# Optimization experiments

Hardware: AMD Instinct MI355X
Metric: run time of the kernel (lower is better)

Reference implementation:

```python
import jax, jax.numpy as jnp
import numpy as np

B, N, C = 8, 4096, 320
HEAD, SR = 5, 2
HEAD_DIM = C // HEAD
SCALE = HEAD_DIM ** -0.5
LN_EPS = 1e-5


def setup_inputs() -> dict:
    key = jax.random.key(0)
    ks = jax.random.split(key, 8)
    s = 0.02
    return {
        "x": jax.random.normal(ks[0], (B, N, C), jnp.float32),
        "q_w": jax.random.normal(ks[1], (C, C), jnp.float32) * s,
        "q_b": jnp.zeros((C,), jnp.float32),
        "kv_w": jax.random.normal(ks[2], (C, 2 * C), jnp.float32) * s,
        "kv_b": jnp.zeros((2 * C,), jnp.float32),
        "sr_w": jax.random.normal(ks[3], (SR, SR, C, C), jnp.float32) * s,  # HWIO
        "sr_b": jnp.zeros((C,), jnp.float32),
        "ln_g": jnp.ones((C,), jnp.float32),
        "ln_b": jnp.zeros((C,), jnp.float32),
        "proj_w": jax.random.normal(ks[4], (C, C), jnp.float32) * s,
        "proj_b": jnp.zeros((C,), jnp.float32),
        "H": 64,
        "W": 64,
    }


def reference(x, q_w, q_b, kv_w, kv_b, sr_w, sr_b, ln_g, ln_b, proj_w, proj_b, H, W):
    b, n, c = x.shape
    # q projection -> [B, head, N, d]
    q = (x @ q_w + q_b).reshape(b, n, HEAD, HEAD_DIM).transpose(0, 2, 1, 3)
    # spatial reduction of KV: strided conv (kernel=stride=SR) + LayerNorm
    x_img = x.reshape(b, H, W, c)  # NHWC
    x_ = jax.lax.conv_general_dilated(
        x_img, sr_w, window_strides=(SR, SR), padding="VALID",
        dimension_numbers=("NHWC", "HWIO", "NHWC")) + sr_b
    x_ = x_.reshape(b, -1, c)  # [B, N/SR^2, C]
    mu = jnp.mean(x_, axis=-1, keepdims=True)
    var = jnp.mean(jnp.square(x_ - mu), axis=-1, keepdims=True)
    x_ = (x_ - mu) * jax.lax.rsqrt(var + LN_EPS) * ln_g + ln_b
    # kv projection -> k, v each [B, head, Nkv, d]
    kv = (x_ @ kv_w + kv_b).reshape(b, -1, 2, HEAD, HEAD_DIM)
    k = kv[:, :, 0].transpose(0, 2, 1, 3)
    v = kv[:, :, 1].transpose(0, 2, 1, 3)
    # attention
    attn = jnp.einsum("bhnd,bhmd->bhnm", q, k) * SCALE
    attn = jax.nn.softmax(attn, axis=-1)
    out = jnp.einsum("bhnm,bhmd->bhnd", attn, v)
    out = out.transpose(0, 2, 1, 3).reshape(b, n, c)
    return out @ proj_w + proj_b
```

## Files before the change

### kernel.cpp

```cpp
#include <hip/hip_runtime.h>

typedef __attribute__((ext_vector_type(8))) short bf16x8;
typedef __attribute__((ext_vector_type(4))) short bf16x4;
typedef __attribute__((ext_vector_type(4))) float f32x4;
typedef __attribute__((ext_vector_type(2))) float f32x2;
typedef __attribute__((ext_vector_type(2))) unsigned u32x2;
typedef __attribute__((ext_vector_type(4))) unsigned u32x4;

#define DEVI static __device__ __forceinline__
#define AS1 __attribute__((address_space(1)))
#define AS3 __attribute__((address_space(3)))

DEVI unsigned short f2bf(float f) {
  unsigned u = __builtin_bit_cast(unsigned, f);
  return (unsigned short)((u + 0x7FFFu + ((u >> 16) & 1u)) >> 16);
}

DEVI unsigned pkbf(float a, float b) {
#if __has_builtin(__builtin_amdgcn_cvt_pk_bf16_f32)
  return __builtin_bit_cast(unsigned, __builtin_amdgcn_cvt_pk_bf16_f32(a, b));
#else
  return (unsigned)f2bf(a) | ((unsigned)f2bf(b) << 16);
#endif
}

DEVI float fast_exp2(float x) {
#if __has_builtin(__builtin_amdgcn_exp2f)
  return __builtin_amdgcn_exp2f(x);
#else
  return exp2f(x);
#endif
}

DEVI void gl_lds16(const unsigned short* g, unsigned short* l) {
  __builtin_amdgcn_global_load_lds((const AS1 unsigned int*)g, (AS3 unsigned int*)l, 16, 0, 0);
}

DEVI size_t frag_off(int row, int k, int KG) {
  return ((size_t)(row >> 4) * KG + (k >> 3)) * 128 + (row & 15) * 8 + (k & 7);
}

__global__ __launch_bounds__(256)
void k_prep(const float* __restrict__ x, unsigned short* __restrict__ xf) {
  __shared__ __align__(16) unsigned short L[20480];
  const int t = threadIdx.x;
  const size_t base = (size_t)blockIdx.x * 64 * 320;
#pragma unroll
  for (int i = 0; i < 10; i++) {
    int c = i * 256 + t;
    const float* p = x + base + (size_t)c * 8;
    f32x4 a = ((const f32x4*)p)[0], b = ((const f32x4*)p)[1];
    u32x4 pk = {pkbf(a[0], a[1]), pkbf(a[2], a[3]), pkbf(b[0], b[1]), pkbf(b[2], b[3])};
    int r = c / 40, g = c - r * 40;
    int gidx = ((r >> 4) * 40 + g) * 16 + (r & 15);
    int sidx = gidx ^ ((gidx >> 4) & 7);
    *(u32x4*)(L + sidx * 8) = pk;
  }
  __syncthreads();
  unsigned short* outb = xf + base;
#pragma unroll
  for (int i = 0; i < 10; i++) {
    int o = i * 256 + t;
    int sidx = o ^ ((o >> 4) & 7);
    *(u32x4*)(outb + (size_t)o * 8) = *(const u32x4*)(L + sidx * 8);
  }
}

__global__ __launch_bounds__(256)
void k_transpose_all(const float* __restrict__ q_w, const float* __restrict__ kv_w,
                     const float* __restrict__ proj_w, const float* __restrict__ sr_w,
                     unsigned short* __restrict__ Wq, unsigned short* __restrict__ Wkv,
                     unsigned short* __restrict__ Wp, unsigned short* __restrict__ Wsr) {
  const float* src; unsigned short* dst; int K, N;
  switch (blockIdx.z) {
    case 0:  src = q_w;    dst = Wq;  K = 320;  N = 320; break;
    case 1:  src = kv_w;   dst = Wkv; K = 320;  N = 640; break;
    case 2:  src = proj_w; dst = Wp;  K = 320;  N = 320; break;
    default: src = sr_w;   dst = Wsr; K = 1280; N = 320; break;
  }
  if ((int)blockIdx.x >= (K >> 5) || (int)blockIdx.y >= (N >> 5)) return;
  const int KG = K >> 3;
  __shared__ float tile[32][33];
  const int k0 = blockIdx.x * 32, n0 = blockIdx.y * 32;
  const int tx = threadIdx.x, ty = threadIdx.y;
#pragma unroll
  for (int i = 0; i < 4; i++)
    tile[ty + i * 8][tx] = src[(size_t)(k0 + ty + i * 8) * N + n0 + tx];
  __syncthreads();
#pragma unroll
  for (int i = 0; i < 4; i++) {
    int n = n0 + ty + i * 8, k = k0 + tx;
    dst[frag_off(n, k, KG)] = f2bf(tile[tx][ty + i * 8]);
  }
}

__global__ __launch_bounds__(256)
void k_ln(const float* __restrict__ xc, const float* __restrict__ gam,
          const float* __restrict__ bet, unsigned short* __restrict__ xr) {
  const int row = blockIdx.x * 4 + (threadIdx.x >> 6);
  const int l = threadIdx.x & 63;
  const float* p = xc + (size_t)row * 320;
  float s = 0.f, ss = 0.f;
#pragma unroll
  for (int i = 0; i < 5; i++) { float v = p[l + 64 * i]; s += v; ss += v * v; }
#pragma unroll
  for (int o = 1; o < 64; o <<= 1) { s += __shfl_xor(s, o); ss += __shfl_xor(ss, o); }
  float mu = s * (1.f / 320.f);
  float var = ss * (1.f / 320.f) - mu * mu;
  float rstd = rsqrtf(var + 1e-5f);
  if (l < 40) {
    f32x4 a = ((const f32x4*)(p + l * 8))[0], b = ((const f32x4*)(p + l * 8))[1];
    f32x4 ga = ((const f32x4*)(gam + l * 8))[0], gb = ((const f32x4*)(gam + l * 8))[1];
    f32x4 ba = ((const f32x4*)(bet + l * 8))[0], bb = ((const f32x4*)(bet + l * 8))[1];
    f32x4 ya, yb;
#pragma unroll
    for (int j = 0; j < 4; j++) {
      ya[j] = (a[j] - mu) * rstd * ga[j] + ba[j];
      yb[j] = (b[j] - mu) * rstd * gb[j] + bb[j];
    }
    u32x4 pk = {pkbf(ya[0], ya[1]), pkbf(ya[2], ya[3]), pkbf(yb[0], yb[1]), pkbf(yb[2], yb[3])};
    *(u32x4*)(xr + ((size_t)((row >> 4) * 40 + l)) * 128 + (row & 15) * 8) = pk;
  }
}

template <int MT, int AK, int EPI, int NSEG>
__global__ __launch_bounds__(256)
void k_gemm(const unsigned short* __restrict__ A, const unsigned short* __restrict__ W,
            const float* __restrict__ bias, void* __restrict__ outp, void* __restrict__ outp2,
            float oscale) {
  __shared__ __align__(16) unsigned short Bl[20480];
  const int t = threadIdx.x, w = t >> 6, ln = t & 63, lr = ln & 15, lq = ln >> 4;
  const int m0 = blockIdx.x * (MT * 64), n0 = blockIdx.y * 64;

  f32x4 acc[MT][4];
#pragma unroll
  for (int i = 0; i < MT; i++)
#pragma unroll
    for (int j = 0; j < 4; j++) acc[i][j] = (f32x4){0.f, 0.f, 0.f, 0.f};

  int crt[MT], crow[MT];
  if (AK == 1) {
#pragma unroll
    for (int mi = 0; mi < MT; mi++) {
      int gm = m0 + (w * MT + mi) * 16;
      int b = gm >> 10, p = gm & 1023, oy = p >> 5, ox0 = p & 31;
      crt[mi] = b * 256 + ((2 * oy) * 64 + 2 * ox0) >> 4;
      crow[mi] = 0;
      (void)crow[mi];
    }
  }

#pragma unroll
  for (int seg = 0; seg < NSEG; seg++) {
    const int kh = seg >> 1, kw = seg & 1;
    if (seg) __syncthreads();
    if (AK == 0) {
      const unsigned short* Ws = W + ((size_t)(n0 >> 4) * 40) * 128;
#pragma unroll
      for (int j = 0; j < 10; j++)
        gl_lds16(Ws + (size_t)(j * 4 + w) * 512 + ln * 8, Bl + (j * 4 + w) * 512);
    } else {
      const unsigned short* Wt = W + ((size_t)((n0 >> 4) + w) * 160 + seg * 40) * 128;
#pragma unroll
      for (int j = 0; j < 10; j++)
        gl_lds16(Wt + (size_t)j * 512 + ln * 8, Bl + w * 5120 + j * 512);
    }
    __syncthreads();

#pragma unroll
    for (int ks = 0; ks < 10; ks++) {
      bf16x8 af[MT], bfr[4];
#pragma unroll
      for (int mi = 0; mi < MT; mi++) {
        if (AK == 0) {
          af[mi] = *(const bf16x8*)(
              A + ((size_t)((m0 >> 4) + w * MT + mi) * 40 + ks * 4 + lq) * 128 + lr * 8);
        } else {
          int gm = m0 + (w * MT + mi) * 16;
          int b = gm >> 10, p = gm & 1023, oy = p >> 5, ox0 = p & 31;
          int r0 = (2 * oy + kh) * 64 + 2 * ox0 + kw;
          int brt = b * 256 + (r0 >> 4);
          af[mi] = *(const bf16x8*)(
              A + ((size_t)(brt + (lr >> 3)) * 40 + ks * 4 + lq) * 128 +
              (kw + 2 * (lr & 7)) * 8);
        }
      }
#pragma unroll
      for (int ni = 0; ni < 4; ni++)
        bfr[ni] = *(const bf16x8*)(Bl + ((ni * 40) + ks * 4 + lq) * 128 + lr * 8);
#pragma unroll
      for (int mi = 0; mi < MT; mi++)
#pragma unroll
        for (int ni = 0; ni < 4; ni++)
          acc[mi][ni] =
              __builtin_amdgcn_mfma_f32_16x16x32_bf16(af[mi], bfr[ni], acc[mi][ni], 0, 0, 0);
    }
  }

  if (EPI == 0) {
    unsigned short* out = (unsigned short*)outp;
    const int h = n0 >> 6;
#pragma unroll
    for (int mi = 0; mi < MT; mi++)
#pragma unroll
      for (int ni = 0; ni < 4; ni++)
#pragma unroll
        for (int rr = 0; rr < 4; rr++) {
          int gm = m0 + (w * MT + mi) * 16 + lq * 4 + rr;
          int b = gm >> 12, n = gm & 4095, d = ni * 16 + lr;
          out[((size_t)(b * 5 + h) << 18) + ((size_t)n << 6) + d] =
              f2bf((acc[mi][ni][rr] + bias[n0 + d]) * oscale);
        }
  } else if (EPI == 3) {
    float* out = (float*)outp;
#pragma unroll
    for (int mi = 0; mi < MT; mi++)
#pragma unroll
      for (int ni = 0; ni < 4; ni++)
#pragma unroll
        for (int rr = 0; rr < 4; rr++) {
          int gm = m0 + (w * MT + mi) * 16 + lq * 4 + rr;
          int gc = n0 + ni * 16 + lr;
          out[(size_t)gm * 320 + gc] = acc[mi][ni][rr] + bias[gc];
        }
  } else {
    if (n0 < 320) {
      unsigned short* out = (unsigned short*)outp;
      const int h = n0 >> 6;
#pragma unroll
      for (int mi = 0; mi < MT; mi++)
#pragma unroll
        for (int ni = 0; ni < 4; ni++)
#pragma unroll
          for (int rr = 0; rr < 4; rr++) {
            int gm = m0 + (w * MT + mi) * 16 + lq * 4 + rr;
            int b = gm >> 10, mm = gm & 1023, d = ni * 16 + lr;
            out[((size_t)(b * 5 + h) << 16) + ((size_t)mm << 6) + d] =
                f2bf(acc[mi][ni][rr] + bias[n0 + d]);
          }
    } else {
      unsigned short* out = (unsigned short*)outp2;
      const int h = (n0 - 320) >> 6;
      unsigned short* Tl = (unsigned short*)Bl;
      __syncthreads();
#pragma unroll
      for (int mi = 0; mi < MT; mi++)
#pragma unroll
        for (int ni = 0; ni < 4; ni++)
#pragma unroll
          for (int rr = 0; rr < 4; rr++) {
            int ml = (w * MT + mi) * 16 + lq * 4 + rr;
            int d = ni * 16 + lr;
            Tl[d * 136 + ml] = f2bf(acc[mi][ni][rr] + bias[n0 + d]);
          }
      __syncthreads();
      const int b = m0 >> 10, mm0 = m0 & 1023;
#pragma unroll
      for (int i = 0; i < 4; i++) {
        int ch = t + 256 * i, d = ch >> 4, g = ch & 15;
        *(bf16x8*)(out + ((size_t)(b * 5 + h) << 16) + d * 1024 + mm0 + g * 8) =
            *(const bf16x8*)(Tl + d * 136 + g * 8);
      }
    }
  }
}

__global__ __launch_bounds__(256)
void k_attn(const unsigned short* __restrict__ Qb, const unsigned short* __restrict__ Kb,
            const unsigned short* __restrict__ Vt, unsigned short* __restrict__ AO) {
  __shared__ __align__(16) unsigned char smem[32768];
  const int t = threadIdx.x, w = t >> 6, ln = t & 63, lr = ln & 15, lq = ln >> 4;
  const int bh = blockIdx.y;
  const int m0 = blockIdx.x * 128 + w * 32;
  const unsigned short* Qp = Qb + ((size_t)bh << 18);
  const unsigned short* Kp = Kb + ((size_t)bh << 16);
  const unsigned short* Vp = Vt + ((size_t)bh << 16);

  bf16x8 qf[2][2];
#pragma unroll
  for (int mt = 0; mt < 2; mt++)
#pragma unroll
    for (int t2 = 0; t2 < 2; t2++)
      qf[mt][t2] = *(const bf16x8*)(Qp + (size_t)(m0 + mt * 16 + lr) * 64 + t2 * 32 + lq * 8);

  f32x4 oacc[4][2];
  f32x2 den2[2] = {(f32x2){0.f, 0.f}, (f32x2){0.f, 0.f}};
#pragma unroll
  for (int dt = 0; dt < 4; dt++)
#pragma unroll
    for (int mt = 0; mt < 2; mt++) oacc[dt][mt] = (f32x4){0.f, 0.f, 0.f, 0.f};

  const int rS = ln >> 3, sS = ln & 7;

  auto stage = [&](int c, int buf) {
    unsigned short* KL = (unsigned short*)(smem + buf * 16384);
    unsigned short* VL = KL + 4096;
#pragma unroll
    for (int i = 0; i < 2; i++) {
      int r = (w * 2 + i) * 8 + rS;
      int g = sS ^ (r & 7);
      gl_lds16(Kp + (size_t)(c * 64 + r) * 64 + g * 8, KL + (w * 2 + i) * 512);
      gl_lds16(Vp + (size_t)r * 1024 + c * 64 + g * 8, VL + (w * 2 + i) * 512);
    }
  };

  stage(0, 0);
  __syncthreads();

  for (int c = 0; c < 16; c++) {
    if (c < 15) stage(c + 1, (c + 1) & 1);
    const unsigned short* KL = (const unsigned short*)(smem + (c & 1) * 16384);
    const unsigned short* VL = KL + 4096;

    f32x4 sacc[4][2];
#pragma unroll
    for (int kt = 0; kt < 4; kt++) {
      int kr = 16 * kt + lr;
      bf16x8 kf0 = *(const bf16x8*)(KL + kr * 64 + ((lq ^ (lr & 7)) * 8));
      bf16x8 kf1 = *(const bf16x8*)(KL + kr * 64 + (((4 + lq) ^ (lr & 7)) * 8));
#pragma unroll
      for (int mt = 0; mt < 2; mt++) {
        f32x4 s = (f32x4){0.f, 0.f, 0.f, 0.f};
        s = __builtin_amdgcn_mfma_f32_16x16x32_bf16(kf0, qf[mt][0], s, 0, 0, 0);
        s = __builtin_amdgcn_mfma_f32_16x16x32_bf16(kf1, qf[mt][1], s, 0, 0, 0);
        sacc[kt][mt] = s;
      }
    }

#pragma unroll
    for (int tp = 0; tp < 2; tp++) {
      bf16x8 pf8[2];
#pragma unroll
      for (int mt = 0; mt < 2; mt++) {
        f32x4 ea, eb;
#pragma unroll
        for (int j = 0; j < 4; j++) {
          ea[j] = fast_exp2(sacc[2 * tp][mt][j]);
          eb[j] = fast_exp2(sacc[2 * tp + 1][mt][j]);
        }
        den2[mt] += (f32x2){ea[0], ea[1]} + (f32x2){ea[2], ea[3]};
        den2[mt] += (f32x2){eb[0], eb[1]} + (f32x2){eb[2], eb[3]};
        u32x4 pk = {pkbf(ea[0], ea[1]), pkbf(ea[2], ea[3]),
                    pkbf(eb[0], eb[1]), pkbf(eb[2], eb[3])};
        pf8[mt] = __builtin_bit_cast(bf16x8, pk);
      }
#pragma unroll
      for (int dt = 0; dt < 4; dt++) {
        int vr = dt * 16 + lr;
        const unsigned short* vbase = VL + vr * 64;
        int ga = 4 * tp + (lq >> 1), gb = ga + 2;
        bf16x4 vlo = *(const bf16x4*)(vbase + (ga ^ (lr & 7)) * 8 + (lq & 1) * 4);
        bf16x4 vhi = *(const bf16x4*)(vbase + (gb ^ (lr & 7)) * 8 + (lq & 1) * 4);
        bf16x8 vf8 = {vlo[0], vlo[1], vlo[2], vlo[3], vhi[0], vhi[1], vhi[2], vhi[3]};
#pragma unroll
        for (int mt = 0; mt < 2; mt++)
          oacc[dt][mt] =
              __builtin_amdgcn_mfma_f32_16x16x32_bf16(vf8, pf8[mt], oacc[dt][mt], 0, 0, 0);
      }
    }
    __syncthreads();
  }

  float inv[2];
#pragma unroll
  for (int mt = 0; mt < 2; mt++) {
    float s = den2[mt][0] + den2[mt][1];
    s += __shfl_xor(s, 16);
    s += __shfl_xor(s, 32);
    inv[mt] = 1.f / s;
  }

  const int b = bh / 5, h = bh - b * 5;
  const int rt0 = b * 256 + (m0 >> 4);
#pragma unroll
  for (int mt = 0; mt < 2; mt++)
#pragma unroll
    for (int dt = 0; dt < 4; dt++) {
      float i0 = inv[mt];
      u32x2 pk = {pkbf(oacc[dt][mt][0] * i0, oacc[dt][mt][1] * i0),
                  pkbf(oacc[dt][mt][2] * i0, oacc[dt][mt][3] * i0)};
      int colg = h * 8 + dt * 2 + (lq >> 1);
      size_t off = ((size_t)(rt0 + mt) * 40 + colg) * 128 + lr * 8 + (lq & 1) * 4;
      *(u32x2*)(AO + off) = pk;
    }
}

extern "C" void kernel_launch(void* const* d_in, const int* in_sizes, int n_in,
                              void* d_out, int out_size, void* d_ws, size_t ws_size,
                              hipStream_t stream) {
  (void)in_sizes; (void)n_in; (void)out_size; (void)ws_size;
  const float* x      = (const float*)d_in[0];
  const float* q_w    = (const float*)d_in[1];
  const float* q_b    = (const float*)d_in[2];
  const float* kv_w   = (const float*)d_in[3];
  const float* kv_b   = (const float*)d_in[4];
  const float* sr_w   = (const float*)d_in[5];
  const float* sr_b   = (const float*)d_in[6];
  const float* ln_g   = (const float*)d_in[7];
  const float* ln_b   = (const float*)d_in[8];
  const float* proj_w = (const float*)d_in[9];
  const float* proj_b = (const float*)d_in[10];
  float* out = (float*)d_out;

  char* ws = (char*)d_ws;
  size_t off = 0;
  auto alloc = [&](size_t bytes) {
    void* p = ws + off;
    off += (bytes + 255) & ~(size_t)255;
    return p;
  };
  unsigned short* xbf_fr = (unsigned short*)alloc((size_t)32768 * 320 * 2);
  unsigned short* Qb     = (unsigned short*)alloc((size_t)32768 * 320 * 2);
  unsigned short* KbP    = (unsigned short*)alloc((size_t)40 * 65536 * 2);
  unsigned short* VtP    = (unsigned short*)alloc((size_t)40 * 65536 * 2);
  float*          xc     = (float*)alloc((size_t)8192 * 320 * 4);
  unsigned short* xr     = (unsigned short*)alloc((size_t)8192 * 320 * 2);
  unsigned short* Wq_fr  = (unsigned short*)alloc((size_t)320 * 320 * 2);
  unsigned short* Wkv_fr = (unsigned short*)alloc((size_t)640 * 320 * 2);
  unsigned short* Wp_fr  = (unsigned short*)alloc((size_t)320 * 320 * 2);
  unsigned short* Wsr_fr = (unsigned short*)alloc((size_t)320 * 1280 * 2);
  unsigned short* AO = xbf_fr;

  const float S2 = 0.125f * 1.4426950408889634f;

  k_prep<<<512, 256, 0, stream>>>(x, xbf_fr);
  k_transpose_all<<<dim3(40, 20, 4), dim3(32, 8), 0, stream>>>(
      q_w, kv_w, proj_w, sr_w, Wq_fr, Wkv_fr, Wp_fr, Wsr_fr);

  k_gemm<2, 1, 3, 4><<<dim3(64, 5), 256, 0, stream>>>(xbf_fr, Wsr_fr, sr_b, xc, nullptr, 1.f);
  k_ln<<<2048, 256, 0, stream>>>(xc, ln_g, ln_b, xr);
  k_gemm<4, 0, 0, 1><<<dim3(128, 5), 256, 0, stream>>>(xbf_fr, Wq_fr, q_b, Qb, nullptr, S2);
  k_gemm<2, 0, 4, 1><<<dim3(64, 10), 256, 0, stream>>>(xr, Wkv_fr, kv_b, KbP, VtP, 1.f);
  k_attn<<<dim3(32, 40), 256, 0, stream>>>(Qb, KbP, VtP, AO);
  k_gemm<4, 0, 3, 1><<<dim3(128, 5), 256, 0, stream>>>(AO, Wp_fr, proj_b, out, nullptr, 1.f);
}
```

Before: 233.1 us.

## Store V in MFMA fragment order and load K/V directly in attention

The KV GEMM epilogue now writes V pre-arranged in the per-lane MFMA operand order. The attention kernel then drops its LDS double-buffer staging and barriers and loads K and V fragments straight from global memory (L2-resident, shared across the 32 query blocks per head). The Q and output projection GEMMs also switch to smaller M tiles with twice as many blocks. The risk is exposed global load latency with no software pipelining, and redundant global traffic across the waves that read the same K/V.

```diff
diff --git a/kernel.cpp b/kernel.cpp
--- a/kernel.cpp
+++ b/kernel.cpp
@@ -137,18 +137,6 @@
   for (int i = 0; i < MT; i++)
 #pragma unroll
     for (int j = 0; j < 4; j++) acc[i][j] = (f32x4){0.f, 0.f, 0.f, 0.f};
-
-  int crt[MT], crow[MT];
-  if (AK == 1) {
-#pragma unroll
-    for (int mi = 0; mi < MT; mi++) {
-      int gm = m0 + (w * MT + mi) * 16;
-      int b = gm >> 10, p = gm & 1023, oy = p >> 5, ox0 = p & 31;
-      crt[mi] = b * 256 + ((2 * oy) * 64 + 2 * ox0) >> 4;
-      crow[mi] = 0;
-      (void)crow[mi];
-    }
-  }
 
 #pragma unroll
   for (int seg = 0; seg < NSEG; seg++) {
@@ -241,7 +229,7 @@
     } else {
       unsigned short* out = (unsigned short*)outp2;
       const int h = (n0 - 320) >> 6;
-      unsigned short* Tl = (unsigned short*)Bl;
+      unsigned short* Tl = Bl;
       __syncthreads();
 #pragma unroll
       for (int mi = 0; mi < MT; mi++)
@@ -254,12 +242,18 @@
             Tl[d * 136 + ml] = f2bf(acc[mi][ni][rr] + bias[n0 + d]);
           }
       __syncthreads();
-      const int b = m0 >> 10, mm0 = m0 & 1023;
-#pragma unroll
-      for (int i = 0; i < 4; i++) {
-        int ch = t + 256 * i, d = ch >> 4, g = ch & 15;
-        *(bf16x8*)(out + ((size_t)(b * 5 + h) << 16) + d * 1024 + mm0 + g * 8) =
-            *(const bf16x8*)(Tl + d * 136 + g * 8);
+      const int b = m0 >> 10, c0 = (m0 & 1023) >> 6, bh = b * 5 + h;
+      const int c2 = w >> 1, tp = w & 1;
+      const int kvl = c2 * 64 + tp * 32 + lq * 4;
+      unsigned short* ob =
+          out + ((size_t)bh << 16) + ((size_t)((c0 + c2) * 8 + tp * 4)) * 512 + ln * 8;
+#pragma unroll
+      for (int dt = 0; dt < 4; dt++) {
+        const unsigned short* tr = Tl + (dt * 16 + lr) * 136 + kvl;
+        bf16x4 lo = *(const bf16x4*)tr;
+        bf16x4 hi = *(const bf16x4*)(tr + 16);
+        bf16x8 v8 = {lo[0], lo[1], lo[2], lo[3], hi[0], hi[1], hi[2], hi[3]};
+        *(bf16x8*)(ob + dt * 512) = v8;
       }
     }
   }
@@ -267,14 +261,13 @@
 
 __global__ __launch_bounds__(256)
 void k_attn(const unsigned short* __restrict__ Qb, const unsigned short* __restrict__ Kb,
-            const unsigned short* __restrict__ Vt, unsigned short* __restrict__ AO) {
-  __shared__ __align__(16) unsigned char smem[32768];
+            const unsigned short* __restrict__ Vf, unsigned short* __restrict__ AO) {
   const int t = threadIdx.x, w = t >> 6, ln = t & 63, lr = ln & 15, lq = ln >> 4;
   const int bh = blockIdx.y;
   const int m0 = blockIdx.x * 128 + w * 32;
   const unsigned short* Qp = Qb + ((size_t)bh << 18);
   const unsigned short* Kp = Kb + ((size_t)bh << 16);
-  const unsigned short* Vp = Vt + ((size_t)bh << 16);
+  const unsigned short* Vp = Vf + ((size_t)bh << 16);
 
   bf16x8 qf[2][2];
 #pragma unroll
@@ -290,53 +283,42 @@
 #pragma unroll
     for (int mt = 0; mt < 2; mt++) oacc[dt][mt] = (f32x4){0.f, 0.f, 0.f, 0.f};
 
-  const int rS = ln >> 3, sS = ln & 7;
-
-  auto stage = [&](int c, int buf) {
-    unsigned short* KL = (unsigned short*)(smem + buf * 16384);
-    unsigned short* VL = KL + 4096;
-#pragma unroll
-    for (int i = 0; i < 2; i++) {
-      int r = (w * 2 + i) * 8 + rS;
-      int g = sS ^ (r & 7);
-      gl_lds16(Kp + (size_t)(c * 64 + r) * 64 + g * 8, KL + (w * 2 + i) * 512);
-      gl_lds16(Vp + (size_t)r * 1024 + c * 64 + g * 8, VL + (w * 2 + i) * 512);
-    }
-  };
-
-  stage(0, 0);
-  __syncthreads();
+  const unsigned short* kc = Kp + lr * 64 + lq * 8;
+  const unsigned short* vc = Vp + ln * 8;
 
   for (int c = 0; c < 16; c++) {
-    if (c < 15) stage(c + 1, (c + 1) & 1);
-    const unsigned short* KL = (const unsigned short*)(smem + (c & 1) * 16384);
-    const unsigned short* VL = KL + 4096;
-
-    f32x4 sacc[4][2];
-#pragma unroll
-    for (int kt = 0; kt < 4; kt++) {
-      int kr = 16 * kt + lr;
-      bf16x8 kf0 = *(const bf16x8*)(KL + kr * 64 + ((lq ^ (lr & 7)) * 8));
-      bf16x8 kf1 = *(const bf16x8*)(KL + kr * 64 + (((4 + lq) ^ (lr & 7)) * 8));
-#pragma unroll
-      for (int mt = 0; mt < 2; mt++) {
-        f32x4 s = (f32x4){0.f, 0.f, 0.f, 0.f};
-        s = __builtin_amdgcn_mfma_f32_16x16x32_bf16(kf0, qf[mt][0], s, 0, 0, 0);
-        s = __builtin_amdgcn_mfma_f32_16x16x32_bf16(kf1, qf[mt][1], s, 0, 0, 0);
-        sacc[kt][mt] = s;
-      }
-    }
-
-#pragma unroll
-    for (int tp = 0; tp < 2; tp++) {
+#pragma unroll
+    for (int hf = 0; hf < 2; hf++) {
+      bf16x8 kfr[2][2], vfr[4];
+#pragma unroll
+      for (int kt2 = 0; kt2 < 2; kt2++)
+#pragma unroll
+        for (int t2 = 0; t2 < 2; t2++)
+          kfr[kt2][t2] =
+              *(const bf16x8*)(kc + c * 4096 + (hf * 2 + kt2) * 1024 + t2 * 32);
+#pragma unroll
+      for (int dt = 0; dt < 4; dt++)
+        vfr[dt] = *(const bf16x8*)(vc + c * 4096 + (hf * 4 + dt) * 512);
+
+      f32x4 sacc[2][2];
+#pragma unroll
+      for (int kt2 = 0; kt2 < 2; kt2++)
+#pragma unroll
+        for (int mt = 0; mt < 2; mt++) {
+          f32x4 s = (f32x4){0.f, 0.f, 0.f, 0.f};
+          s = __builtin_amdgcn_mfma_f32_16x16x32_bf16(kfr[kt2][0], qf[mt][0], s, 0, 0, 0);
+          s = __builtin_amdgcn_mfma_f32_16x16x32_bf16(kfr[kt2][1], qf[mt][1], s, 0, 0, 0);
+          sacc[kt2][mt] = s;
+        }
+
       bf16x8 pf8[2];
 #pragma unroll
       for (int mt = 0; mt < 2; mt++) {
         f32x4 ea, eb;
 #pragma unroll
         for (int j = 0; j < 4; j++) {
-          ea[j] = fast_exp2(sacc[2 * tp][mt][j]);
-          eb[j] = fast_exp2(sacc[2 * tp + 1][mt][j]);
+          ea[j] = fast_exp2(sacc[0][mt][j]);
+          eb[j] = fast_exp2(sacc[1][mt][j]);
         }
         den2[mt] += (f32x2){ea[0], ea[1]} + (f32x2){ea[2], ea[3]};
         den2[mt] += (f32x2){eb[0], eb[1]} + (f32x2){eb[2], eb[3]};
@@ -344,21 +326,14 @@
                     pkbf(eb[0], eb[1]), pkbf(eb[2], eb[3])};
         pf8[mt] = __builtin_bit_cast(bf16x8, pk);
       }
-#pragma unroll
-      for (int dt = 0; dt < 4; dt++) {
-        int vr = dt * 16 + lr;
-        const unsigned short* vbase = VL + vr * 64;
-        int ga = 4 * tp + (lq >> 1), gb = ga + 2;
-        bf16x4 vlo = *(const bf16x4*)(vbase + (ga ^ (lr & 7)) * 8 + (lq & 1) * 4);
-        bf16x4 vhi = *(const bf16x4*)(vbase + (gb ^ (lr & 7)) * 8 + (lq & 1) * 4);
-        bf16x8 vf8 = {vlo[0], vlo[1], vlo[2], vlo[3], vhi[0], vhi[1], vhi[2], vhi[3]};
+
+#pragma unroll
+      for (int dt = 0; dt < 4; dt++)
 #pragma unroll
         for (int mt = 0; mt < 2; mt++)
           oacc[dt][mt] =
-              __builtin_amdgcn_mfma_f32_16x16x32_bf16(vf8, pf8[mt], oacc[dt][mt], 0, 0, 0);
-      }
-    }
-    __syncthreads();
+              __builtin_amdgcn_mfma_f32_16x16x32_bf16(vfr[dt], pf8[mt], oacc[dt][mt], 0, 0, 0);
+    }
   }
 
   float inv[2];
@@ -412,7 +387,7 @@
   unsigned short* xbf_fr = (unsigned short*)alloc((size_t)32768 * 320 * 2);
   unsigned short* Qb     = (unsigned short*)alloc((size_t)32768 * 320 * 2);
   unsigned short* KbP    = (unsigned short*)alloc((size_t)40 * 65536 * 2);
-  unsigned short* VtP    = (unsigned short*)alloc((size_t)40 * 65536 * 2);
+  unsigned short* VfP    = (unsigned short*)alloc((size_t)40 * 65536 * 2);
   float*          xc     = (float*)alloc((size_t)8192 * 320 * 4);
   unsigned short* xr     = (unsigned short*)alloc((size_t)8192 * 320 * 2);
   unsigned short* Wq_fr  = (unsigned short*)alloc((size_t)320 * 320 * 2);
@@ -429,8 +404,8 @@
 
   k_gemm<2, 1, 3, 4><<<dim3(64, 5), 256, 0, stream>>>(xbf_fr, Wsr_fr, sr_b, xc, nullptr, 1.f);
   k_ln<<<2048, 256, 0, stream>>>(xc, ln_g, ln_b, xr);
-  k_gemm<4, 0, 0, 1><<<dim3(128, 5), 256, 0, stream>>>(xbf_fr, Wq_fr, q_b, Qb, nullptr, S2);
-  k_gemm<2, 0, 4, 1><<<dim3(64, 10), 256, 0, stream>>>(xr, Wkv_fr, kv_b, KbP, VtP, 1.f);
-  k_attn<<<dim3(32, 40), 256, 0, stream>>>(Qb, KbP, VtP, AO);
-  k_gemm<4, 0, 3, 1><<<dim3(128, 5), 256, 0, stream>>>(AO, Wp_fr, proj_b, out, nullptr, 1.f);
-}
+  k_gemm<2, 0, 0, 1><<<dim3(256, 5), 256, 0, stream>>>(xbf_fr, Wq_fr, q_b, Qb, nullptr, S2);
+  k_gemm<2, 0, 4, 1><<<dim3(64, 10), 256, 0, stream>>>(xr, Wkv_fr, kv_b, KbP, VfP, 1.f);
+  k_attn<<<dim3(32, 40), 256, 0, stream>>>(Qb, KbP, VfP, AO);
+  k_gemm<2, 0, 3, 1><<<dim3(256, 5), 256, 0, stream>>>(AO, Wp_fr, proj_b, out, nullptr, 1.f);
+}
```

Measured after the change: 278.4 us. 1.19x slower.
